# Kernel tuning notes

Measured on AMD Instinct MI355X. Metric: run time of the kernel, lower is better.

Reference implementation:

```python
import jax, jax.numpy as jnp
import numpy as np


def setup_inputs() -> dict:
    key = jax.random.key(0)
    ks = jax.random.split(key, 8)
    T, B, O, H, A = 512, 256, 720, 128, 2
    s = lambda k, shp, sc: (jax.random.normal(k, shp, jnp.float32) * sc)
    return {
        "x": jax.random.normal(ks[0], (T, B, O), jnp.float32),
        "h0": jnp.zeros((B, H), jnp.float32),
        "c0": jnp.zeros((B, H), jnp.float32),
        "Wx": s(ks[1], (O, 4 * H), 1.0 / np.sqrt(O)),
        "Wh": s(ks[2], (H, 4 * H), 1.0 / np.sqrt(H)),
        "b": jnp.zeros((4 * H,), jnp.float32),
        "Wa1": s(ks[3], (H, H), np.sqrt(2.0 / H)),
        "ba1": jnp.zeros((H,), jnp.float32),
        "Wa2": s(ks[4], (H, A), 0.01),
        "ba2": jnp.zeros((A,), jnp.float32),
        "log_std": jnp.zeros((A,), jnp.float32),
        "Wc1": s(ks[5], (H, H), np.sqrt(2.0 / H)),
        "bc1": jnp.zeros((H,), jnp.float32),
        "Wc2": s(ks[6], (H, 1), 0.01),
        "bc2": jnp.zeros((1,), jnp.float32),
    }


def _lstm(x, h0, c0, Wx, Wh, b):
    # Precompute input projections for all timesteps: [T, B, 4H]
    xW = jnp.einsum('tbo,og->tbg', x, Wx) + b

    def step(carry, xw_t):
        h, c = carry
        gates = xw_t + h @ Wh  # [B, 4H]
        i, f, g, o = jnp.split(gates, 4, axis=-1)
        c = jax.nn.sigmoid(f) * c + jax.nn.sigmoid(i) * jnp.tanh(g)
        h = jax.nn.sigmoid(o) * jnp.tanh(c)
        return (h, c), h

    (hT, cT), _ = jax.lax.scan(step, (h0, c0), xW)
    return hT, cT


def reference(x, h0, c0, Wx, Wh, b, Wa1, ba1, Wa2, ba2, log_std,
              Wc1, bc1, Wc2, bc2):
    hT, cT = _lstm(x, h0, c0, Wx, Wh, b)
    feat = hT  # outputs[-1] == last hidden state (unidirectional)
    actor_mean = jnp.tanh(feat @ Wa1 + ba1) @ Wa2 + ba2  # [B, A]
    std = jnp.exp(log_std)  # [A]
    value = (jnp.tanh(feat @ Wc1 + bc1) @ Wc2 + bc2).squeeze(-1)  # [B]
    return actor_mean, std, value, hT, cT
```

## Files before the change

kernel.cpp:

```cpp
#include <hip/hip_runtime.h>
#include <hip/hip_bf16.h>

typedef unsigned int   u32;
typedef unsigned short u16;
typedef _Float16       f16;
typedef __attribute__((ext_vector_type(8))) _Float16 f16x8;
typedef __attribute__((ext_vector_type(4))) float    f32x4;

#define T_STEPS 512
#define BATCH   256
#define O_IN    720
#define KPAD    736
#define HID     128
#define G4      512
#define OUT_STD 512
#define OUT_VAL 514
#define OUT_HT  770
#define OUT_CT  33538

static const unsigned long long XW_OFF  = 0ull;
static const unsigned long long WXT_OFF = 134217728ull;

__device__ inline float exp2fast(float x){
#if __has_builtin(__builtin_amdgcn_exp2f)
  return __builtin_amdgcn_exp2f(x);
#else
  return exp2f(x);
#endif
}
__device__ inline float sigf(float x){ return 1.0f / (1.0f + exp2fast(-1.44269504f * x)); }
__device__ inline float tanhfast(float x){ return 2.0f / (1.0f + exp2fast(-2.88539008f * x)) - 1.0f; }

__global__ void k_pack_wxt(const float* __restrict__ Wx, u16* __restrict__ wxt){
  const int n = blockIdx.x;
  for (int k = threadIdx.x; k < KPAD; k += 256){
    float v = (k < O_IN) ? Wx[(size_t)k * G4 + n] : 0.f;
    wxt[(size_t)n * KPAD + k] = __builtin_bit_cast(u16, (f16)v);
  }
}

__global__ __launch_bounds__(256, 2) void k_gemm(const float* __restrict__ x,
                                                 const u16* __restrict__ wxt,
                                                 u16* __restrict__ xw)
{
  const int l  = threadIdx.x & 63;
  const int w  = threadIdx.x >> 6;
  const int lr = l & 15;
  const int lk = l >> 4;
  const u32 L  = (blockIdx.x & 7u) * 256u + (blockIdx.x >> 3);
  const u32 mb = L >> 2, nb = L & 3u;
  const u32 M0 = mb * 256u + (u32)w * 64u;
  const u32 N0 = nb * 128u;

  const float* ax[4];
  const u16*   bx[8];
#pragma unroll
  for (int mf = 0; mf < 4; ++mf)
    ax[mf] = x + (unsigned long long)(M0 + mf*16 + lr) * O_IN + lk*8;
#pragma unroll
  for (int nf = 0; nf < 8; ++nf)
    bx[nf] = wxt + (unsigned long long)(N0 + nf*16 + lr) * KPAD + lk*8;

  f32x4 acc[4][8];
#pragma unroll
  for (int mf = 0; mf < 4; ++mf)
#pragma unroll
    for (int nf = 0; nf < 8; ++nf)
      acc[mf][nf] = (f32x4){0.f, 0.f, 0.f, 0.f};

  f32x4 a0[4][2];
  f16x8 aF[4], bF[8];

#pragma unroll
  for (int mf = 0; mf < 4; ++mf){
    a0[mf][0] = *(const f32x4*)(ax[mf]);
    a0[mf][1] = *(const f32x4*)(ax[mf] + 4);
  }
#pragma unroll
  for (int nf = 0; nf < 8; ++nf)
    bF[nf] = *(const f16x8*)(bx[nf]);
#pragma unroll
  for (int mf = 0; mf < 4; ++mf){
    f32x4 lo = a0[mf][0], hi = a0[mf][1];
    f16x8 v; v[0]=(f16)lo.x; v[1]=(f16)lo.y; v[2]=(f16)lo.z; v[3]=(f16)lo.w;
             v[4]=(f16)hi.x; v[5]=(f16)hi.y; v[6]=(f16)hi.z; v[7]=(f16)hi.w;
    aF[mf] = v;
  }

  for (int kc = 0; kc < 22; ++kc){
    if (kc < 21){
#pragma unroll
      for (int mf = 0; mf < 4; ++mf){
        a0[mf][0] = *(const f32x4*)(ax[mf] + (kc+1)*32);
        a0[mf][1] = *(const f32x4*)(ax[mf] + (kc+1)*32 + 4);
      }
    }
#pragma unroll
    for (int nf = 0; nf < 8; ++nf){
#pragma unroll
      for (int mf = 0; mf < 4; ++mf)
        acc[mf][nf] = __builtin_amdgcn_mfma_f32_16x16x32_f16(aF[mf], bF[nf], acc[mf][nf], 0, 0, 0);
      if (kc < 21)
        bF[nf] = *(const f16x8*)(bx[nf] + (kc+1)*32);
    }
    if (kc < 21){
#pragma unroll
      for (int mf = 0; mf < 4; ++mf){
        f32x4 lo = a0[mf][0], hi = a0[mf][1];
        f16x8 v; v[0]=(f16)lo.x; v[1]=(f16)lo.y; v[2]=(f16)lo.z; v[3]=(f16)lo.w;
                 v[4]=(f16)hi.x; v[5]=(f16)hi.y; v[6]=(f16)hi.z; v[7]=(f16)hi.w;
        aF[mf] = v;
      }
    }
  }

  {
    f16x8 aT[4];
#pragma unroll
    for (int mf = 0; mf < 4; ++mf) aT[mf] = (f16x8)(f16)0.f;
    if (lk < 2){
#pragma unroll
      for (int mf = 0; mf < 4; ++mf){
        f32x4 lo = *(const f32x4*)(ax[mf] + 704);
        f32x4 hi = *(const f32x4*)(ax[mf] + 708);
        f16x8 v; v[0]=(f16)lo.x; v[1]=(f16)lo.y; v[2]=(f16)lo.z; v[3]=(f16)lo.w;
                 v[4]=(f16)hi.x; v[5]=(f16)hi.y; v[6]=(f16)hi.z; v[7]=(f16)hi.w;
        aT[mf] = v;
      }
    }
#pragma unroll
    for (int nf = 0; nf < 8; ++nf){
      f16x8 bT = *(const f16x8*)(bx[nf] + 704);
#pragma unroll
      for (int mf = 0; mf < 4; ++mf)
        acc[mf][nf] = __builtin_amdgcn_mfma_f32_16x16x32_f16(aT[mf], bT, acc[mf][nf], 0, 0, 0);
    }
  }

#pragma unroll
  for (int mf = 0; mf < 4; ++mf){
    const u32 rowb = M0 + mf*16 + lk*4;
#pragma unroll
    for (int nf = 0; nf < 8; ++nf){
      const u32 col = N0 + nf*16 + lr;
#pragma unroll
      for (int r = 0; r < 4; ++r)
        xw[(unsigned long long)(rowb + r) * G4 + col] = __builtin_bit_cast(u16, (f16)acc[mf][nf][r]);
    }
  }
}

__global__ __launch_bounds__(512) void k_rnn(
    const u16* __restrict__ xw, const float* __restrict__ Wh,
    const float* __restrict__ h0, const float* __restrict__ c0,
    const float* __restrict__ bvec,
    const float* __restrict__ Wa1, const float* __restrict__ ba1,
    const float* __restrict__ Wa2, const float* __restrict__ ba2,
    const float* __restrict__ Wc1, const float* __restrict__ bc1,
    const float* __restrict__ Wc2, const float* __restrict__ bc2,
    const float* __restrict__ log_std, float* __restrict__ out)
{
  const int b = blockIdx.x;
  const int t = threadIdx.x;

  __shared__ __align__(16) float hf[HID];
  __shared__ float act[G4];
  __shared__ float hid[256];

  float w[HID];
#pragma unroll
  for (int k = 0; k < HID; ++k)
    w[k] = Wh[(u32)k * G4 + t];
  const float bb = bvec[t];

  float cs = 0.f, hv = 0.f;
  if (t < HID){
    hv = h0[b*HID + t];
    cs = c0[b*HID + t];
    hf[t] = hv;
  }
  __syncthreads();

  const u16* xp = xw + (u32)b * G4 + t;
  u16 xcur = xp[0];
  const bool is_g = ((t >> 7) == 2);
  const f32x4* hp4 = (const f32x4*)hf;

  for (int s = 0; s < T_STEPS; ++s){
    u16 xnext = 0;
    if (s + 1 < T_STEPS) xnext = xp[(u32)(s+1) * 131072u];

    float s0 = 0.f, s1 = 0.f, s2 = 0.f, s3 = 0.f;
#pragma unroll
    for (int q = 0; q < 32; ++q){
      f32x4 hh = hp4[q];
      s0 = fmaf(hh.x, w[4*q+0], s0);
      s1 = fmaf(hh.y, w[4*q+1], s1);
      s2 = fmaf(hh.z, w[4*q+2], s2);
      s3 = fmaf(hh.w, w[4*q+3], s3);
    }
    float g = (float)__builtin_bit_cast(f16, xcur) + bb + ((s0 + s1) + (s2 + s3));
    act[t] = is_g ? tanhfast(g) : sigf(g);
    __syncthreads();
    if (t < HID){
      float gi = act[t], gf = act[t + 128], gg = act[t + 256], go = act[t + 384];
      cs = gf * cs + gi * gg;
      hv = go * tanhfast(cs);
      hf[t] = hv;
    }
    __syncthreads();
    xcur = xnext;
  }

  if (t < HID){
    out[OUT_HT + b*HID + t] = hv;
    out[OUT_CT + b*HID + t] = cs;
  }

  if (t < 256){
    const float* W = (t < HID) ? Wa1 : Wc1;
    const int col  = t & (HID - 1);
    float a0 = 0.f, a1 = 0.f, a2 = 0.f, a3 = 0.f;
#pragma unroll
    for (int q = 0; q < 32; ++q){
      f32x4 hh = hp4[q];
      a0 = fmaf(hh.x, W[(u32)(4*q+0)*HID + col], a0);
      a1 = fmaf(hh.y, W[(u32)(4*q+1)*HID + col], a1);
      a2 = fmaf(hh.z, W[(u32)(4*q+2)*HID + col], a2);
      a3 = fmaf(hh.w, W[(u32)(4*q+3)*HID + col], a3);
    }
    float a = (a0 + a1) + (a2 + a3);
    hid[t] = (t < HID) ? tanhfast(a + ba1[col]) : tanhfast(a + bc1[col]);
  }
  __syncthreads();

  {
    const int wv = t >> 6, lane = t & 63;
    float p = 0.f;
    if (wv == 0)      p = hid[lane]     * Wa2[lane*2]   + hid[lane+64]     * Wa2[(lane+64)*2];
    else if (wv == 1) p = hid[lane]     * Wa2[lane*2+1] + hid[lane+64]     * Wa2[(lane+64)*2+1];
    else if (wv == 2) p = hid[128+lane] * Wc2[lane]     + hid[128+lane+64] * Wc2[lane+64];
#pragma unroll
    for (int off = 32; off > 0; off >>= 1) p += __shfl_down(p, off);
    if (lane == 0){
      if (wv == 0) out[b*2 + 0]   = p + ba2[0];
      if (wv == 1) out[b*2 + 1]   = p + ba2[1];
      if (wv == 2) out[OUT_VAL+b] = p + bc2[0];
    }
    if (b == 0 && wv == 3 && lane < 2) out[OUT_STD + lane] = expf(log_std[lane]);
  }
}

extern "C" void kernel_launch(void* const* d_in, const int* in_sizes, int n_in,
                              void* d_out, int out_size, void* d_ws, size_t ws_size,
                              hipStream_t stream)
{
  (void)in_sizes; (void)n_in; (void)out_size; (void)ws_size;
  const float* x    = (const float*)d_in[0];
  const float* h0   = (const float*)d_in[1];
  const float* c0   = (const float*)d_in[2];
  const float* Wx   = (const float*)d_in[3];
  const float* Wh   = (const float*)d_in[4];
  const float* bv   = (const float*)d_in[5];
  const float* Wa1  = (const float*)d_in[6];
  const float* ba1  = (const float*)d_in[7];
  const float* Wa2  = (const float*)d_in[8];
  const float* ba2  = (const float*)d_in[9];
  const float* lstd = (const float*)d_in[10];
  const float* Wc1  = (const float*)d_in[11];
  const float* bc1  = (const float*)d_in[12];
  const float* Wc2  = (const float*)d_in[13];
  const float* bc2  = (const float*)d_in[14];
  float* out = (float*)d_out;
  char*  ws  = (char*)d_ws;

  u16* xw  = (u16*)(ws + XW_OFF);
  u16* wxt = (u16*)(ws + WXT_OFF);

  k_pack_wxt<<<dim3(512),  dim3(256), 0, stream>>>(Wx, wxt);
  k_gemm<<<dim3(2048),     dim3(256), 0, stream>>>(x, wxt, xw);
  k_rnn<<<dim3(256),       dim3(512), 0, stream>>>(xw, Wh, h0, c0, bv,
                                                   Wa1, ba1, Wa2, ba2, Wc1, bc1, Wc2, bc2,
                                                   lstd, out);
}
```

Baseline: 727.2 us.

## Batch 16 sequences per block and run recurrent matmul on MFMA

The recurrent kernel now gives each block 16 batch rows and computes h@Wh with fp16 MFMA, keeping Wh in registers as fp16 fragments. The GEMM folds the bias into the projection and stores its output in MFMA fragment order, so each step loads accumulator initial values directly. This cuts the grid from 256 blocks to 16, trading fewer busy CUs for much denser per-step compute. It also lowers precision, since h and Wh are now fp16 in the recurrence, and the 16-step sequential critical path per block gets longer.

```diff
diff --git a/kernel.cpp b/kernel.cpp
--- a/kernel.cpp
+++ b/kernel.cpp
@@ -4,8 +4,10 @@
 typedef unsigned int   u32;
 typedef unsigned short u16;
 typedef _Float16       f16;
+typedef __attribute__((ext_vector_type(2))) _Float16 f16x2;
 typedef __attribute__((ext_vector_type(8))) _Float16 f16x8;
 typedef __attribute__((ext_vector_type(4))) float    f32x4;
+typedef __attribute__((ext_vector_type(2))) float    f32x2;
 
 #define T_STEPS 512
 #define BATCH   256
@@ -31,6 +33,12 @@
 __device__ inline float sigf(float x){ return 1.0f / (1.0f + exp2fast(-1.44269504f * x)); }
 __device__ inline float tanhfast(float x){ return 2.0f / (1.0f + exp2fast(-2.88539008f * x)) - 1.0f; }
 
+__device__ inline u32 pkf16(float a, float b){
+  f16x2 p; p[0] = (f16)a; p[1] = (f16)b; return __builtin_bit_cast(u32, p);
+}
+__device__ inline float lo16f(u32 u){ return (float)__builtin_bit_cast(f16, (u16)(u & 0xffffu)); }
+__device__ inline float hi16f(u32 u){ return (float)__builtin_bit_cast(f16, (u16)(u >> 16)); }
+
 __global__ void k_pack_wxt(const float* __restrict__ Wx, u16* __restrict__ wxt){
   const int n = blockIdx.x;
   for (int k = threadIdx.x; k < KPAD; k += 256){
@@ -41,7 +49,8 @@
 
 __global__ __launch_bounds__(256, 2) void k_gemm(const float* __restrict__ x,
                                                  const u16* __restrict__ wxt,
-                                                 u16* __restrict__ xw)
+                                                 const float* __restrict__ bvec,
+                                                 u16* __restrict__ xwf)
 {
   const int l  = threadIdx.x & 63;
   const int w  = threadIdx.x >> 6;
@@ -137,118 +146,163 @@
     }
   }
 
+  float bs[8];
+#pragma unroll
+  for (int nf = 0; nf < 8; ++nf) bs[nf] = bvec[N0 + nf*16 + lr];
 #pragma unroll
   for (int mf = 0; mf < 4; ++mf){
-    const u32 rowb = M0 + mf*16 + lk*4;
 #pragma unroll
     for (int nf = 0; nf < 8; ++nf){
-      const u32 col = N0 + nf*16 + lr;
-#pragma unroll
-      for (int r = 0; r < 4; ++r)
-        xw[(unsigned long long)(rowb + r) * G4 + col] = __builtin_bit_cast(u16, (f16)acc[mf][nf][r]);
-    }
-  }
-}
-
-__global__ __launch_bounds__(512) void k_rnn(
-    const u16* __restrict__ xw, const float* __restrict__ Wh,
+      f32x4 a = acc[mf][nf];
+      uint2 v;
+      v.x = pkf16(a[0] + bs[nf], a[1] + bs[nf]);
+      v.y = pkf16(a[2] + bs[nf], a[3] + bs[nf]);
+      unsigned long long off =
+        ((unsigned long long)(mb*16u + 4u*(u32)w + (u32)mf) * 32u + (nb*8u + (u32)nf)) * 512ull
+        + (unsigned long long)l * 8ull;
+      *(uint2*)((char*)xwf + off) = v;
+    }
+  }
+}
+
+__global__ __launch_bounds__(1024, 1) void k_rnn(
+    const u16* __restrict__ xwf, const float* __restrict__ Wh,
     const float* __restrict__ h0, const float* __restrict__ c0,
-    const float* __restrict__ bvec,
     const float* __restrict__ Wa1, const float* __restrict__ ba1,
     const float* __restrict__ Wa2, const float* __restrict__ ba2,
     const float* __restrict__ Wc1, const float* __restrict__ bc1,
     const float* __restrict__ Wc2, const float* __restrict__ bc2,
     const float* __restrict__ log_std, float* __restrict__ out)
 {
-  const int b = blockIdx.x;
-  const int t = threadIdx.x;
-
-  __shared__ __align__(16) float hf[HID];
-  __shared__ float act[G4];
-  __shared__ float hid[256];
-
-  float w[HID];
-#pragma unroll
-  for (int k = 0; k < HID; ++k)
-    w[k] = Wh[(u32)k * G4 + t];
-  const float bb = bvec[t];
-
-  float cs = 0.f, hv = 0.f;
-  if (t < HID){
-    hv = h0[b*HID + t];
-    cs = c0[b*HID + t];
-    hf[t] = hv;
-  }
+  const int b0 = blockIdx.x;
+  const int t  = threadIdx.x;
+  const int w  = t >> 6;
+  const int l  = t & 63;
+  const int lr = l & 15;
+  const int g4 = l >> 4;
+
+  __shared__ __align__(16) u16   h16[16 * 136];
+  __shared__ __align__(16) float act[16 * 516];
+  __shared__ __align__(16) float hfin[16 * 128];
+  __shared__ float hid2[16 * 256];
+
+  f16x8 wb[4][2];
+  {
+    const int col0 = 32*w + lr;
+#pragma unroll
+    for (int nf2 = 0; nf2 < 2; ++nf2){
+      const int col = col0 + 16*nf2;
+#pragma unroll
+      for (int kk = 0; kk < 4; ++kk){
+        f16x8 v;
+#pragma unroll
+        for (int j = 0; j < 8; ++j)
+          v[j] = (f16)Wh[(u32)(kk*32 + g4*8 + j) * G4 + col];
+        wb[kk][nf2] = v;
+      }
+    }
+  }
+
+  const int bb = b0*16 + w;
+  float c0v = c0[bb*HID + 2*l], c1v = c0[bb*HID + 2*l + 1];
+  float h0v = h0[bb*HID + 2*l], h1v = h0[bb*HID + 2*l + 1];
+  *(u32*)((char*)h16 + w*272 + l*4) = pkf16(h0v, h1v);
   __syncthreads();
 
-  const u16* xp = xw + (u32)b * G4 + t;
-  u16 xcur = xp[0];
-  const bool is_g = ((t >> 7) == 2);
-  const f32x4* hp4 = (const f32x4*)hf;
+  const char* xp = (const char*)xwf
+                 + ((unsigned long long)b0 * 32u + 2u*(u32)w) * 512ull + (u32)l * 8u;
+  uint2 xq0 = *(const uint2*)(xp);
+  uint2 xq1 = *(const uint2*)(xp + 512);
+  const u32 region = (u32)w >> 2;
 
   for (int s = 0; s < T_STEPS; ++s){
-    u16 xnext = 0;
-    if (s + 1 < T_STEPS) xnext = xp[(u32)(s+1) * 131072u];
-
-    float s0 = 0.f, s1 = 0.f, s2 = 0.f, s3 = 0.f;
-#pragma unroll
-    for (int q = 0; q < 32; ++q){
-      f32x4 hh = hp4[q];
-      s0 = fmaf(hh.x, w[4*q+0], s0);
-      s1 = fmaf(hh.y, w[4*q+1], s1);
-      s2 = fmaf(hh.z, w[4*q+2], s2);
-      s3 = fmaf(hh.w, w[4*q+3], s3);
-    }
-    float g = (float)__builtin_bit_cast(f16, xcur) + bb + ((s0 + s1) + (s2 + s3));
-    act[t] = is_g ? tanhfast(g) : sigf(g);
+    f16x8 af[4];
+#pragma unroll
+    for (int kk = 0; kk < 4; ++kk)
+      af[kk] = *(const f16x8*)((const char*)h16 + lr*272 + kk*64 + g4*16);
+
+    uint2 xn0, xn1; xn0.x=xn0.y=xn1.x=xn1.y=0u;
+    if (s + 1 < T_STEPS){
+      const char* xnp = xp + (u32)(s+1) * 262144u;
+      xn0 = *(const uint2*)(xnp);
+      xn1 = *(const uint2*)(xnp + 512);
+    }
+
+    f32x4 acc0, acc1;
+    acc0 = (f32x4){lo16f(xq0.x), hi16f(xq0.x), lo16f(xq0.y), hi16f(xq0.y)};
+    acc1 = (f32x4){lo16f(xq1.x), hi16f(xq1.x), lo16f(xq1.y), hi16f(xq1.y)};
+#pragma unroll
+    for (int kk = 0; kk < 4; ++kk){
+      acc0 = __builtin_amdgcn_mfma_f32_16x16x32_f16(af[kk], wb[kk][0], acc0, 0, 0, 0);
+      acc1 = __builtin_amdgcn_mfma_f32_16x16x32_f16(af[kk], wb[kk][1], acc1, 0, 0, 0);
+    }
+
+#pragma unroll
+    for (int rr = 0; rr < 4; ++rr){
+      float* ap = act + (g4*4 + rr)*516 + 32*w + lr;
+      float v0 = acc0[rr], v1 = acc1[rr];
+      if (region == 2){ v0 = tanhfast(v0); v1 = tanhfast(v1); }
+      else            { v0 = sigf(v0);     v1 = sigf(v1);     }
+      ap[0]  = v0;
+      ap[16] = v1;
+    }
     __syncthreads();
-    if (t < HID){
-      float gi = act[t], gf = act[t + 128], gg = act[t + 256], go = act[t + 384];
-      cs = gf * cs + gi * gg;
-      hv = go * tanhfast(cs);
-      hf[t] = hv;
+    {
+      const float* ar = act + w*516 + 2*l;
+      f32x2 gi = *(const f32x2*)(ar);
+      f32x2 gf = *(const f32x2*)(ar + 128);
+      f32x2 gg = *(const f32x2*)(ar + 256);
+      f32x2 go = *(const f32x2*)(ar + 384);
+      c0v = gf.x*c0v + gi.x*gg.x;
+      c1v = gf.y*c1v + gi.y*gg.y;
+      h0v = go.x*tanhfast(c0v);
+      h1v = go.y*tanhfast(c1v);
+      *(u32*)((char*)h16 + w*272 + l*4) = pkf16(h0v, h1v);
     }
     __syncthreads();
-    xcur = xnext;
-  }
-
-  if (t < HID){
-    out[OUT_HT + b*HID + t] = hv;
-    out[OUT_CT + b*HID + t] = cs;
-  }
-
-  if (t < 256){
-    const float* W = (t < HID) ? Wa1 : Wc1;
-    const int col  = t & (HID - 1);
-    float a0 = 0.f, a1 = 0.f, a2 = 0.f, a3 = 0.f;
-#pragma unroll
-    for (int q = 0; q < 32; ++q){
-      f32x4 hh = hp4[q];
-      a0 = fmaf(hh.x, W[(u32)(4*q+0)*HID + col], a0);
-      a1 = fmaf(hh.y, W[(u32)(4*q+1)*HID + col], a1);
-      a2 = fmaf(hh.z, W[(u32)(4*q+2)*HID + col], a2);
-      a3 = fmaf(hh.w, W[(u32)(4*q+3)*HID + col], a3);
-    }
-    float a = (a0 + a1) + (a2 + a3);
-    hid[t] = (t < HID) ? tanhfast(a + ba1[col]) : tanhfast(a + bc1[col]);
-  }
+    xq0 = xn0; xq1 = xn1;
+  }
+
+  f32x2 hvv; hvv.x = h0v; hvv.y = h1v;
+  f32x2 cvv; cvv.x = c0v; cvv.y = c1v;
+  *(f32x2*)(out + OUT_HT + bb*HID + 2*l) = hvv;
+  *(f32x2*)(out + OUT_CT + bb*HID + 2*l) = cvv;
+  *(f32x2*)(hfin + w*HID + 2*l) = hvv;
   __syncthreads();
 
   {
-    const int wv = t >> 6, lane = t & 63;
-    float p = 0.f;
-    if (wv == 0)      p = hid[lane]     * Wa2[lane*2]   + hid[lane+64]     * Wa2[(lane+64)*2];
-    else if (wv == 1) p = hid[lane]     * Wa2[lane*2+1] + hid[lane+64]     * Wa2[(lane+64)*2+1];
-    else if (wv == 2) p = hid[128+lane] * Wc2[lane]     + hid[128+lane+64] * Wc2[lane+64];
-#pragma unroll
-    for (int off = 32; off > 0; off >>= 1) p += __shfl_down(p, off);
-    if (lane == 0){
-      if (wv == 0) out[b*2 + 0]   = p + ba2[0];
-      if (wv == 1) out[b*2 + 1]   = p + ba2[1];
-      if (wv == 2) out[OUT_VAL+b] = p + bc2[0];
-    }
-    if (b == 0 && wv == 3 && lane < 2) out[OUT_STD + lane] = expf(log_std[lane]);
-  }
+    const int hc  = t & 255;
+    const int r2  = t >> 8;
+    const float* W = (hc < HID) ? Wa1 : Wc1;
+    const int col = hc & (HID-1);
+    float a0=0.f, a1=0.f, a2=0.f, a3=0.f;
+    for (int k = 0; k < HID; ++k){
+      float wv = W[(u32)k*HID + col];
+      a0 = fmaf(hfin[(r2     )*HID + k], wv, a0);
+      a1 = fmaf(hfin[(r2 + 4 )*HID + k], wv, a1);
+      a2 = fmaf(hfin[(r2 + 8 )*HID + k], wv, a2);
+      a3 = fmaf(hfin[(r2 + 12)*HID + k], wv, a3);
+    }
+    float bsv = (hc < HID) ? ba1[col] : bc1[col];
+    hid2[(r2     )*256 + hc] = tanhfast(a0 + bsv);
+    hid2[(r2 + 4 )*256 + hc] = tanhfast(a1 + bsv);
+    hid2[(r2 + 8 )*256 + hc] = tanhfast(a2 + bsv);
+    hid2[(r2 + 12)*256 + hc] = tanhfast(a3 + bsv);
+  }
+  __syncthreads();
+
+  if (t < 48){
+    const int a = t >> 4, r = t & 15;
+    float s = 0.f;
+    if (a < 2){
+      for (int k = 0; k < HID; ++k) s = fmaf(hid2[r*256 + k], Wa2[k*2 + a], s);
+      out[(b0*16 + r)*2 + a] = s + ba2[a];
+    } else {
+      for (int k = 0; k < HID; ++k) s = fmaf(hid2[r*256 + 128 + k], Wc2[k], s);
+      out[OUT_VAL + b0*16 + r] = s + bc2[0];
+    }
+  }
+  if (b0 == 0 && t >= 64 && t < 66) out[OUT_STD + (t - 64)] = expf(log_std[t - 64]);
 }
 
 extern "C" void kernel_launch(void* const* d_in, const int* in_sizes, int n_in,
@@ -274,12 +328,12 @@
   float* out = (float*)d_out;
   char*  ws  = (char*)d_ws;
 
-  u16* xw  = (u16*)(ws + XW_OFF);
+  u16* xwf = (u16*)(ws + XW_OFF);
   u16* wxt = (u16*)(ws + WXT_OFF);
 
-  k_pack_wxt<<<dim3(512),  dim3(256), 0, stream>>>(Wx, wxt);
-  k_gemm<<<dim3(2048),     dim3(256), 0, stream>>>(x, wxt, xw);
-  k_rnn<<<dim3(256),       dim3(512), 0, stream>>>(xw, Wh, h0, c0, bv,
-                                                   Wa1, ba1, Wa2, ba2, Wc1, bc1, Wc2, bc2,
-                                                   lstd, out);
-}
+  k_pack_wxt<<<dim3(512),  dim3(256),  0, stream>>>(Wx, wxt);
+  k_gemm<<<dim3(2048),     dim3(256),  0, stream>>>(x, wxt, bv, xwf);
+  k_rnn<<<dim3(16),        dim3(1024), 0, stream>>>(xwf, Wh, h0, c0,
+                                                    Wa1, ba1, Wa2, ba2, Wc1, bc1, Wc2, bc2,
+                                                    lstd, out);
+}
```

New measurement: 1.155 ms. 1.59x slower.

## Split recurrent matvec over K with shuffle reductions and double-buffered hidden state

Applied to the files above, without the earlier changes.

Reorganizes the per-step LSTM recurrence so each group of four threads owns one hidden unit. Each thread computes all four gate partial sums over a quarter of K, then the group reduces and exchanges gate activations with warp shuffles. The activation shared-memory array and one of the two per-step barriers go away, with h double-buffered in padded LDS to reduce bank conflicts. The price is more shuffles per step and the same 128 weight registers per thread, now split into four arrays.

```diff
diff --git a/kernel.cpp b/kernel.cpp
--- a/kernel.cpp
+++ b/kernel.cpp
@@ -30,6 +30,10 @@
 }
 __device__ inline float sigf(float x){ return 1.0f / (1.0f + exp2fast(-1.44269504f * x)); }
 __device__ inline float tanhfast(float x){ return 2.0f / (1.0f + exp2fast(-2.88539008f * x)) - 1.0f; }
+
+#define HQ_STRIDE 144
+#define H_BYTES   (4*HQ_STRIDE)
+#define HOFF(j)   ((j)*4 + ((j)>>5)*16)
 
 __global__ void k_pack_wxt(const float* __restrict__ Wx, u16* __restrict__ wxt){
   const int n = blockIdx.x;
@@ -162,72 +166,97 @@
 {
   const int b = blockIdx.x;
   const int t = threadIdx.x;
-
+  const int j = t >> 2;
+  const int q = t & 3;
+  const int l = t & 63;
+  const int lbase = l & ~3;
+
+  __shared__ __align__(16) char hbuf[2][H_BYTES];
   __shared__ __align__(16) float hf[HID];
-  __shared__ float act[G4];
   __shared__ float hid[256];
 
-  float w[HID];
-#pragma unroll
-  for (int k = 0; k < HID; ++k)
-    w[k] = Wh[(u32)k * G4 + t];
-  const float bb = bvec[t];
-
-  float cs = 0.f, hv = 0.f;
-  if (t < HID){
-    hv = h0[b*HID + t];
-    cs = c0[b*HID + t];
-    hf[t] = hv;
-  }
+  float w0[32], w1[32], w2[32], w3[32];
+#pragma unroll
+  for (int kk = 0; kk < 32; ++kk){
+    const u32 krow = (u32)(32*q + kk) * G4 + (u32)j;
+    w0[kk] = Wh[krow];
+    w1[kk] = Wh[krow + 128];
+    w2[kk] = Wh[krow + 256];
+    w3[kk] = Wh[krow + 384];
+  }
+  const float bb = bvec[j + 128*q];
+
+  float cs = c0[b*HID + j];
+  float hv = h0[b*HID + j];
+  if (q == 0)
+    *(float*)(hbuf[0] + HOFF(j)) = hv;
   __syncthreads();
 
-  const u16* xp = xw + (u32)b * G4 + t;
-  u16 xcur = xp[0];
-  const bool is_g = ((t >> 7) == 2);
-  const f32x4* hp4 = (const f32x4*)hf;
+  const u16* xp = xw + (u32)b * G4 + (u32)(j + 128*q);
+  float xc  = (float)__builtin_bit_cast(f16, xp[0]) + bb;
+  float xn1 = (T_STEPS > 1) ? (float)__builtin_bit_cast(f16, xp[131072u]) + bb : 0.f;
 
   for (int s = 0; s < T_STEPS; ++s){
-    u16 xnext = 0;
-    if (s + 1 < T_STEPS) xnext = xp[(u32)(s+1) * 131072u];
-
-    float s0 = 0.f, s1 = 0.f, s2 = 0.f, s3 = 0.f;
-#pragma unroll
-    for (int q = 0; q < 32; ++q){
-      f32x4 hh = hp4[q];
-      s0 = fmaf(hh.x, w[4*q+0], s0);
-      s1 = fmaf(hh.y, w[4*q+1], s1);
-      s2 = fmaf(hh.z, w[4*q+2], s2);
-      s3 = fmaf(hh.w, w[4*q+3], s3);
-    }
-    float g = (float)__builtin_bit_cast(f16, xcur) + bb + ((s0 + s1) + (s2 + s3));
-    act[t] = is_g ? tanhfast(g) : sigf(g);
+    const char* hq = hbuf[s & 1] + q * HQ_STRIDE;
+
+    float xn2 = 0.f;
+    if (s + 2 < T_STEPS)
+      xn2 = (float)__builtin_bit_cast(f16, xp[(u32)(s+2) * 131072u]) + bb;
+
+    float p0 = 0.f, p1 = 0.f, p2 = 0.f, p3 = 0.f;
+#pragma unroll
+    for (int it = 0; it < 8; ++it){
+      f32x4 hh = *(const f32x4*)(hq + it*16);
+      p0 = fmaf(hh.x, w0[4*it+0], p0);  p0 = fmaf(hh.y, w0[4*it+1], p0);
+      p0 = fmaf(hh.z, w0[4*it+2], p0);  p0 = fmaf(hh.w, w0[4*it+3], p0);
+      p1 = fmaf(hh.x, w1[4*it+0], p1);  p1 = fmaf(hh.y, w1[4*it+1], p1);
+      p1 = fmaf(hh.z, w1[4*it+2], p1);  p1 = fmaf(hh.w, w1[4*it+3], p1);
+      p2 = fmaf(hh.x, w2[4*it+0], p2);  p2 = fmaf(hh.y, w2[4*it+1], p2);
+      p2 = fmaf(hh.z, w2[4*it+2], p2);  p2 = fmaf(hh.w, w2[4*it+3], p2);
+      p3 = fmaf(hh.x, w3[4*it+0], p3);  p3 = fmaf(hh.y, w3[4*it+1], p3);
+      p3 = fmaf(hh.z, w3[4*it+2], p3);  p3 = fmaf(hh.w, w3[4*it+3], p3);
+    }
+    p0 += __shfl_xor(p0, 1);  p1 += __shfl_xor(p1, 1);
+    p2 += __shfl_xor(p2, 1);  p3 += __shfl_xor(p3, 1);
+    p0 += __shfl_xor(p0, 2);  p1 += __shfl_xor(p1, 2);
+    p2 += __shfl_xor(p2, 2);  p3 += __shfl_xor(p3, 2);
+
+    float gsum = (q == 0) ? p0 : (q == 1) ? p1 : (q == 2) ? p2 : p3;
+    float gval = gsum + xc;
+    float av   = (q == 2) ? tanhfast(gval) : sigf(gval);
+
+    float ai = __shfl(av, lbase + 0);
+    float af = __shfl(av, lbase + 1);
+    float ag = __shfl(av, lbase + 2);
+    float ao = __shfl(av, lbase + 3);
+
+    cs = af * cs + ai * ag;
+    hv = ao * tanhfast(cs);
+    if (q == 0)
+      *(float*)(hbuf[(s & 1) ^ 1] + HOFF(j)) = hv;
     __syncthreads();
-    if (t < HID){
-      float gi = act[t], gf = act[t + 128], gg = act[t + 256], go = act[t + 384];
-      cs = gf * cs + gi * gg;
-      hv = go * tanhfast(cs);
-      hf[t] = hv;
-    }
-    __syncthreads();
-    xcur = xnext;
-  }
-
-  if (t < HID){
-    out[OUT_HT + b*HID + t] = hv;
-    out[OUT_CT + b*HID + t] = cs;
-  }
+    xc = xn1; xn1 = xn2;
+  }
+
+  if (q == 0){
+    out[OUT_HT + b*HID + j] = hv;
+    out[OUT_CT + b*HID + j] = cs;
+    hf[j] = hv;
+  }
+  __syncthreads();
 
   if (t < 256){
     const float* W = (t < HID) ? Wa1 : Wc1;
     const int col  = t & (HID - 1);
+    const f32x4* hp4 = (const f32x4*)hf;
     float a0 = 0.f, a1 = 0.f, a2 = 0.f, a3 = 0.f;
 #pragma unroll
-    for (int q = 0; q < 32; ++q){
-      f32x4 hh = hp4[q];
-      a0 = fmaf(hh.x, W[(u32)(4*q+0)*HID + col], a0);
-      a1 = fmaf(hh.y, W[(u32)(4*q+1)*HID + col], a1);
-      a2 = fmaf(hh.z, W[(u32)(4*q+2)*HID + col], a2);
-      a3 = fmaf(hh.w, W[(u32)(4*q+3)*HID + col], a3);
+    for (int qq = 0; qq < 32; ++qq){
+      f32x4 hh = hp4[qq];
+      a0 = fmaf(hh.x, W[(u32)(4*qq+0)*HID + col], a0);
+      a1 = fmaf(hh.y, W[(u32)(4*qq+1)*HID + col], a1);
+      a2 = fmaf(hh.z, W[(u32)(4*qq+2)*HID + col], a2);
+      a3 = fmaf(hh.w, W[(u32)(4*qq+3)*HID + col], a3);
     }
     float a = (a0 + a1) + (a2 + a3);
     hid[t] = (t < HID) ? tanhfast(a + ba1[col]) : tanhfast(a + bc1[col]);
```

Measured after the change: 863.6 us. 1.19x slower.
